# Performance work log

Measured on AMD Instinct MI355X. Metric: run time of the kernel, lower is better.

Reference implementation:

```python
import jax, jax.numpy as jnp
import numpy as np

B, T, E, H = 64, 200, 512, 8
D = E // H          # head size 64
SCALE = E ** -0.5   # NOTE: original scales by EMBED_DIM**-0.5, not head_size**-0.5


def _ln(x, g, b):
    mu = jnp.mean(x, axis=-1, keepdims=True)
    d = x - mu
    v = jnp.mean(d * d, axis=-1, keepdims=True)
    return g * d * jax.lax.rsqrt(v + 1e-5) + b


def _forward(idx, memory, src_mask, pred_mask,
             sa_wq, sa_wk, sa_wv, sa_wo, sa_bo,
             ca_wq, ca_wk, ca_wv, ca_wo, ca_bo,
             f_w1, f_b1, f_w2, f_b2,
             ln1_g, ln1_b, ln2_g, ln2_b, ln3_g, ln3_b):
    causal = jnp.tril(jnp.ones((T, T), dtype=bool))      # [T,T]
    pm = (pred_mask != 0)[:, None, :, None]              # [B,1,T,1]
    sm = (src_mask != 0)[:, None, :, None]               # [B,1,T,1]

    # --- masked multi-head self-attention (query AND key zeroed by pred_mask) ---
    h = _ln(idx, ln1_g, ln1_b)
    q = jnp.where(pm, jnp.einsum('bte,hed->bhtd', h, sa_wq), 0.0)
    k = jnp.where(pm, jnp.einsum('bte,hed->bhtd', h, sa_wk), 0.0)
    v = jnp.einsum('bte,hed->bhtd', h, sa_wv)
    s = jnp.einsum('bhtd,bhsd->bhts', q, k) * SCALE
    s = jnp.where(causal, s, -jnp.inf)
    w = jax.nn.softmax(s, axis=-1)
    o = jnp.einsum('bhts,bhsd->bthd', w, v).reshape(B, T, E)
    idx = o @ sa_wo + sa_bo + idx

    # --- cross-attention: keys from memory (src-masked), VALUES FROM x (per original code) ---
    h = _ln(idx, ln2_g, ln2_b)
    q = jnp.einsum('bte,hed->bhtd', h, ca_wq)
    k = jnp.where(sm, jnp.einsum('bse,hed->bhsd', memory, ca_wk), 0.0)
    v = jnp.einsum('bte,hed->bhtd', h, ca_wv)
    s = jnp.einsum('bhtd,bhsd->bhts', q, k) * SCALE
    s = jnp.where(causal, s, -jnp.inf)   # mask=True in Decoder's ca
    w = jax.nn.softmax(s, axis=-1)
    o = jnp.einsum('bhts,bhsd->bthd', w, v).reshape(B, T, E)
    idx = o @ ca_wo + ca_bo + idx

    # --- feed-forward ---
    h = _ln(idx, ln3_g, ln3_b)
    idx = jax.nn.relu(h @ f_w1 + f_b1) @ f_w2 + f_b2 + idx
    return idx


def setup_inputs() -> dict:
    key = jax.random.key(0)
    ks = jax.random.split(key, 20)
    nrm = lambda k, sh: jax.random.normal(k, sh, jnp.float32) * 0.02
    return {
        'idx': jax.random.normal(ks[0], (B, T, E), jnp.float32),
        'memory': jax.random.normal(ks[1], (B, T, E), jnp.float32),
        'src_mask': jax.random.randint(ks[2], (B, T), 0, 2, jnp.int32),
        'pred_mask': jax.random.randint(ks[3], (B, T), 0, 2, jnp.int32),
        'sa_wq': nrm(ks[4], (H, E, D)), 'sa_wk': nrm(ks[5], (H, E, D)),
        'sa_wv': nrm(ks[6], (H, E, D)),
        'sa_wo': nrm(ks[7], (E, E)), 'sa_bo': jnp.zeros((E,), jnp.float32),
        'ca_wq': nrm(ks[8], (H, E, D)), 'ca_wk': nrm(ks[9], (H, E, D)),
        'ca_wv': nrm(ks[10], (H, E, D)),
        'ca_wo': nrm(ks[11], (E, E)), 'ca_bo': jnp.zeros((E,), jnp.float32),
        'f_w1': nrm(ks[12], (E, 4 * E)), 'f_b1': jnp.zeros((4 * E,), jnp.float32),
        'f_w2': nrm(ks[13], (4 * E, E)), 'f_b2': jnp.zeros((E,), jnp.float32),
        'ln1_g': jnp.ones((E,), jnp.float32), 'ln1_b': jnp.zeros((E,), jnp.float32),
        'ln2_g': jnp.ones((E,), jnp.float32), 'ln2_b': jnp.zeros((E,), jnp.float32),
        'ln3_g': jnp.ones((E,), jnp.float32), 'ln3_b': jnp.zeros((E,), jnp.float32),
    }


def reference(idx, memory, src_mask, pred_mask,
              sa_wq, sa_wk, sa_wv, sa_wo, sa_bo,
              ca_wq, ca_wk, ca_wv, ca_wo, ca_bo,
              f_w1, f_b1, f_w2, f_b2,
              ln1_g, ln1_b, ln2_g, ln2_b, ln3_g, ln3_b):
    return _forward(idx, memory, src_mask, pred_mask,
                    sa_wq, sa_wk, sa_wv, sa_wo, sa_bo,
                    ca_wq, ca_wk, ca_wv, ca_wo, ca_bo,
                    f_w1, f_b1, f_w2, f_b2,
                    ln1_g, ln1_b, ln2_g, ln2_b, ln3_g, ln3_b)
```

## Files before the change

kernel.cpp:

```cpp
#include <hip/hip_runtime.h>
#include <hip/hip_bf16.h>

#define B_ 64
#define T_ 200
#define E_ 512
#define H_ 8
#define D_ 64

static constexpr float SCALE = 0.044194173824159216f;

typedef __attribute__((ext_vector_type(8))) short bf16x8;
typedef __attribute__((ext_vector_type(4))) short bf16x4;
typedef __attribute__((ext_vector_type(4))) float f32x4;

static __device__ inline short f2bf(float f) {
    __hip_bfloat16 h = __float2bfloat16(f);
    return *(short*)&h;
}

static __device__ __forceinline__ void gload16(const short* g, short* l) {
    __builtin_amdgcn_global_load_lds(
        (const __attribute__((address_space(1))) void*)g,
        (__attribute__((address_space(3))) void*)l, 16, 0, 0);
}

__global__ void conv_kernel(const float* __restrict__ in,
                            __hip_bfloat16* __restrict__ out, int n) {
    int i = (blockIdx.x * blockDim.x + threadIdx.x) * 4;
    if (i < n) {
        f32x4 v = *(const f32x4*)(in + i);
        bf16x4 r;
        #pragma unroll
        for (int j = 0; j < 4; ++j) r[j] = f2bf(v[j]);
        *(bf16x4*)((short*)out + i) = r;
    }
}

template <int MODE>
__global__ __launch_bounds__(256) void wt_kernel(const float* __restrict__ in,
                                                 __hip_bfloat16* __restrict__ out,
                                                 int N, int K) {
    __shared__ float tile[64][65];
    int n0 = blockIdx.x * 64, k0 = blockIdx.y * 64;
    int tx = threadIdx.x & 63, ty = threadIdx.x >> 6;
    #pragma unroll
    for (int i = 0; i < 16; ++i) {
        int k = k0 + ty + i * 4;
        float v;
        if (MODE == 0) {
            v = in[(size_t)k * N + n0 + tx];
        } else {
            int h = n0 >> 6;
            v = in[((size_t)h * K + k) * 64 + tx];
        }
        tile[ty + i * 4][tx] = v;
    }
    __syncthreads();
    #pragma unroll
    for (int i = 0; i < 16; ++i) {
        int n = ty + i * 4;
        out[(size_t)(n0 + n) * K + k0 + tx] = __float2bfloat16(tile[tx][n]);
    }
}

__global__ __launch_bounds__(256) void ln_kernel(const float* __restrict__ x,
                                                 const float* __restrict__ g,
                                                 const float* __restrict__ bta,
                                                 __hip_bfloat16* __restrict__ out) {
    __shared__ float red[4];
    int row = blockIdx.x;
    const float* xr = x + (size_t)row * E_;
    int tid = threadIdx.x;
    float v0 = xr[tid], v1 = xr[tid + 256];
    float s = v0 + v1;
    for (int off = 32; off; off >>= 1) s += __shfl_down(s, off, 64);
    if ((tid & 63) == 0) red[tid >> 6] = s;
    __syncthreads();
    float mu = (red[0] + red[1] + red[2] + red[3]) * (1.0f / E_);
    __syncthreads();
    float d0 = v0 - mu, d1 = v1 - mu;
    float sq = d0 * d0 + d1 * d1;
    for (int off = 32; off; off >>= 1) sq += __shfl_down(sq, off, 64);
    if ((tid & 63) == 0) red[tid >> 6] = sq;
    __syncthreads();
    float var = (red[0] + red[1] + red[2] + red[3]) * (1.0f / E_);
    float r = rsqrtf(var + 1e-5f);
    out[(size_t)row * E_ + tid] = __float2bfloat16(g[tid] * d0 * r + bta[tid]);
    out[(size_t)row * E_ + tid + 256] =
        __float2bfloat16(g[tid + 256] * d1 * r + bta[tid + 256]);
}

template <int MSK, int RELU, int OM, int RES, int BIAS>
__global__ __launch_bounds__(256) void mgemm_kernel(
    const short* __restrict__ A, const short* __restrict__ BT,
    const float* __restrict__ bias, const int* __restrict__ rmask,
    const float* __restrict__ resid, void* __restrict__ Cv,
    int M, int N, int K, size_t wstep) {
    __shared__ __align__(16) short As[2][128 * 32];
    __shared__ __align__(16) short Bs[2][128 * 32];
    int tid = threadIdx.x;
    int wave = tid >> 6, lane = tid & 63;
    int qq = lane >> 4, l15 = lane & 15;

    int nwg = gridDim.x * gridDim.y;
    int flat = blockIdx.y * gridDim.x + blockIdx.x;
    int xcd = flat & 7, bix = flat >> 3;
    int qw = nwg >> 3, rw = nwg & 7;
    int nf = (xcd < rw ? xcd * (qw + 1) : rw * (qw + 1) + (xcd - rw) * qw) + bix;
    int by = nf / gridDim.x, bx = nf - by * gridDim.x;
    int m0 = by * 128, n0 = bx * 128;
    int wm = (wave & 1) * 64, wn = (wave >> 1) * 64;

    int srow = lane >> 2;
    int scol = ((lane & 3) ^ ((srow >> 1) & 3)) * 8;
    const short* gA = A + (size_t)(m0 + wave * 32 + srow) * K + scol;
    const short* gB = BT + (size_t)(n0 + wave * 32 + srow) * K + scol;
    int lofs = wave * 1024;
    size_t rstep = (size_t)16 * K;

    int swz = (qq ^ ((l15 >> 1) & 3)) * 8;

    f32x4 acc[4][4] = {};

    gload16(gA, &As[0][lofs]);
    gload16(gA + rstep, &As[0][lofs + 512]);
    gload16(gB, &Bs[0][lofs]);
    gload16(gB + rstep, &Bs[0][lofs + 512]);

    int nk = K >> 5;
    for (int it = 0; it < nk; ++it) {
        int cur = it & 1;
        if (it + 1 < nk) {
            int k1 = (it + 1) << 5;
            int nxt = cur ^ 1;
            gload16(gA + k1, &As[nxt][lofs]);
            gload16(gA + k1 + rstep, &As[nxt][lofs + 512]);
            gload16(gB + k1, &Bs[nxt][lofs]);
            gload16(gB + k1 + rstep, &Bs[nxt][lofs + 512]);
            asm volatile("s_waitcnt vmcnt(4)" ::: "memory");
        } else {
            asm volatile("s_waitcnt vmcnt(0)" ::: "memory");
        }
        __builtin_amdgcn_s_barrier();
        bf16x8 af[4], bfr[4];
        #pragma unroll
        for (int i = 0; i < 4; ++i)
            af[i] = *(bf16x8*)(&As[cur][(wm + i * 16 + l15) * 32 + swz]);
        #pragma unroll
        for (int j = 0; j < 4; ++j)
            bfr[j] = *(bf16x8*)(&Bs[cur][(wn + j * 16 + l15) * 32 + swz]);
        #pragma unroll
        for (int i = 0; i < 4; ++i)
            #pragma unroll
            for (int j = 0; j < 4; ++j)
                acc[i][j] = __builtin_amdgcn_mfma_f32_16x16x32_bf16(
                    af[i], bfr[j], acc[i][j], 0, 0, 0);
        asm volatile("" ::: "memory");
        __builtin_amdgcn_s_barrier();
    }

    #pragma unroll
    for (int i = 0; i < 4; ++i) {
        #pragma unroll
        for (int r = 0; r < 4; ++r) {
            int row = m0 + wm + i * 16 + qq * 4 + r;
            float mval = 1.0f;
            if (MSK) mval = (rmask[row] != 0) ? 1.0f : 0.0f;
            #pragma unroll
            for (int j = 0; j < 4; ++j) {
                int col = n0 + wn + j * 16 + l15;
                float val = acc[i][j][r];
                if (BIAS) val += bias[col];
                if (MSK == 1) val *= mval;
                if (MSK == 2) { if (col < 1024) val *= mval; }
                if (RELU) val = fmaxf(val, 0.0f);
                if (RES) val += resid[(size_t)row * N + col];
                if (OM == 0) {
                    ((float*)Cv)[(size_t)row * N + col] = val;
                } else if (OM == 1) {
                    int b_ = row / T_, t = row - b_ * T_;
                    int hh = col >> 6, d = col & 63;
                    ((__hip_bfloat16*)Cv)[(((size_t)b_ * H_ + hh) * T_ + t) * D_ + d] =
                        __float2bfloat16(val);
                } else if (OM == 3) {
                    int b_ = row / T_, t = row - b_ * T_;
                    int which = col >> 9, cc = col & 511;
                    int hh = cc >> 6, d = cc & 63;
                    ((__hip_bfloat16*)Cv)[(size_t)which * wstep +
                                          (((size_t)b_ * H_ + hh) * T_ + t) * D_ + d] =
                        __float2bfloat16(val);
                } else {
                    ((__hip_bfloat16*)Cv)[(size_t)row * N + col] =
                        __float2bfloat16(val);
                }
            }
        }
    }
}

#define NQT 13
__global__ __launch_bounds__(256) void fattn_kernel(const short* __restrict__ q,
                                                    const short* __restrict__ k,
                                                    const short* __restrict__ v,
                                                    __hip_bfloat16* __restrict__ o) {
    __shared__ __align__(16) short Kf[NQT * 8 * 16 * 8];
    __shared__ __align__(16) short Vf[4 * 28 * 16 * 8];
    __shared__ __align__(16) short Pb[4 * 512];

    int tid = threadIdx.x;
    int wave = tid >> 6, lane = tid & 63;
    int qq = lane >> 4, l15 = lane & 15;
    int bh = blockIdx.x;
    int b = bh >> 3, h = bh & 7;

    const short* kp = k + (size_t)bh * T_ * D_;
    const short* vp = v + (size_t)bh * T_ * D_;
    const short* qp = q + (size_t)bh * T_ * D_;

    for (int idx = tid; idx < 8 * 208; idx += 256) {
        int g = idx / 208, s = idx - g * 208;
        int kt = s >> 4, l = s & 15;
        bf16x8 val;
        if (s < 200) {
            val = *(const bf16x8*)(kp + (size_t)s * 64 + g * 8);
        } else {
            #pragma unroll
            for (int j = 0; j < 8; ++j) val[j] = 0;
        }
        *(bf16x8*)&Kf[((kt * 8 + g) * 16 + l) * 8] = val;
    }
    for (int idx = tid; idx < 28 * 64; idx += 256) {
        int g = idx >> 6, d = idx & 63;
        int nt = d >> 4, dl = d & 15;
        bf16x8 val;
        if (g < 25) {
            #pragma unroll
            for (int j = 0; j < 8; ++j) val[j] = vp[(g * 8 + j) * 64 + d];
        } else {
            #pragma unroll
            for (int j = 0; j < 8; ++j) val[j] = 0;
        }
        *(bf16x8*)&Vf[((nt * 28 + g) * 16 + dl) * 8] = val;
    }
    __syncthreads();

    short* pb = &Pb[wave * 512];

    for (int qt = wave; qt < NQT; qt += 4) {
        int t0 = qt * 16;
        bf16x8 qf[2];
        #pragma unroll
        for (int ks = 0; ks < 2; ++ks)
            qf[ks] = *(const bf16x8*)(qp + (size_t)(t0 + l15) * 64 + ks * 32 + qq * 8);
        f32x4 sc[NQT];
        #pragma unroll
        for (int kt = 0; kt < NQT; ++kt) {
            f32x4 a = {0.f, 0.f, 0.f, 0.f};
            bf16x8 kf0 = *(const bf16x8*)&Kf[((kt * 8 + qq) * 16 + l15) * 8];
            bf16x8 kf1 = *(const bf16x8*)&Kf[((kt * 8 + 4 + qq) * 16 + l15) * 8];
            a = __builtin_amdgcn_mfma_f32_16x16x32_bf16(qf[0], kf0, a, 0, 0, 0);
            a = __builtin_amdgcn_mfma_f32_16x16x32_bf16(qf[1], kf1, a, 0, 0, 0);
            sc[kt] = a;
        }
        #pragma unroll
        for (int kt = 0; kt < NQT; ++kt) {
            #pragma unroll
            for (int r = 0; r < 4; ++r) {
                int col = kt * 16 + l15;
                int rowg = t0 + qq * 4 + r;
                sc[kt][r] = (col <= rowg) ? sc[kt][r] * SCALE : -1e30f;
            }
        }
        float mx[4], sum[4], inv[4];
        #pragma unroll
        for (int r = 0; r < 4; ++r) {
            float m = -1e30f;
            #pragma unroll
            for (int kt = 0; kt < NQT; ++kt) m = fmaxf(m, sc[kt][r]);
            #pragma unroll
            for (int off = 1; off < 16; off <<= 1)
                m = fmaxf(m, __shfl_xor(m, off, 64));
            mx[r] = m;
        }
        #pragma unroll
        for (int r = 0; r < 4; ++r) sum[r] = 0.f;
        #pragma unroll
        for (int kt = 0; kt < NQT; ++kt) {
            #pragma unroll
            for (int r = 0; r < 4; ++r) {
                float e = __expf(sc[kt][r] - mx[r]);
                sc[kt][r] = e;
                sum[r] += e;
            }
        }
        #pragma unroll
        for (int r = 0; r < 4; ++r) {
            float s = sum[r];
            #pragma unroll
            for (int off = 1; off < 16; off <<= 1) s += __shfl_xor(s, off, 64);
            inv[r] = 1.0f / s;
        }
        f32x4 oa[4] = {};
        #pragma unroll
        for (int c = 0; c < 7; ++c) {
            #pragma unroll
            for (int kt2 = 0; kt2 < 2; ++kt2) {
                int kt = c * 2 + kt2;
                int g = kt2 * 2 + (l15 >> 3);
                int jj = l15 & 7;
                #pragma unroll
                for (int r = 0; r < 4; ++r) {
                    float val = (kt < NQT) ? sc[kt][r] : 0.0f;
                    pb[(g * 16 + qq * 4 + r) * 8 + jj] = f2bf(val);
                }
            }
            bf16x8 pf = *(const bf16x8*)&pb[(qq * 16 + l15) * 8];
            #pragma unroll
            for (int nt = 0; nt < 4; ++nt) {
                bf16x8 vf = *(const bf16x8*)&Vf[((nt * 28 + c * 4 + qq) * 16 + l15) * 8];
                oa[nt] = __builtin_amdgcn_mfma_f32_16x16x32_bf16(pf, vf, oa[nt], 0, 0, 0);
            }
        }
        #pragma unroll
        for (int nt = 0; nt < 4; ++nt) {
            #pragma unroll
            for (int r = 0; r < 4; ++r) {
                int t = t0 + qq * 4 + r;
                if (t < T_) {
                    int d = nt * 16 + l15;
                    o[((size_t)b * T_ + t) * E_ + h * D_ + d] =
                        __float2bfloat16(oa[nt][r] * inv[r]);
                }
            }
        }
    }
}

extern "C" void kernel_launch(void* const* d_in, const int* in_sizes, int n_in,
                              void* d_out, int out_size, void* d_ws, size_t ws_size,
                              hipStream_t stream) {
    const float* idx    = (const float*)d_in[0];
    const float* memory = (const float*)d_in[1];
    const int* src_mask  = (const int*)d_in[2];
    const int* pred_mask = (const int*)d_in[3];
    const float* sa_wq = (const float*)d_in[4];
    const float* sa_wk = (const float*)d_in[5];
    const float* sa_wv = (const float*)d_in[6];
    const float* sa_wo = (const float*)d_in[7];
    const float* sa_bo = (const float*)d_in[8];
    const float* ca_wq = (const float*)d_in[9];
    const float* ca_wk = (const float*)d_in[10];
    const float* ca_wv = (const float*)d_in[11];
    const float* ca_wo = (const float*)d_in[12];
    const float* ca_bo = (const float*)d_in[13];
    const float* f_w1  = (const float*)d_in[14];
    const float* f_b1  = (const float*)d_in[15];
    const float* f_w2  = (const float*)d_in[16];
    const float* f_b2  = (const float*)d_in[17];
    const float* ln1_g = (const float*)d_in[18];
    const float* ln1_b = (const float*)d_in[19];
    const float* ln2_g = (const float*)d_in[20];
    const float* ln2_b = (const float*)d_in[21];
    const float* ln3_g = (const float*)d_in[22];
    const float* ln3_b = (const float*)d_in[23];
    float* out = (float*)d_out;

    const size_t BTE = (size_t)B_ * T_ * E_;
    const size_t EE = (size_t)E_ * E_;

    char* p = (char*)d_ws;
    short* qb = (short*)p;            p += BTE * 2;
    short* kb = (short*)p;            p += BTE * 2;
    short* vb = (short*)p;            p += BTE * 2;
    float* x1 = (float*)p;            p += BTE * 4;
    __hip_bfloat16* h_bf   = (__hip_bfloat16*)p; p += BTE * 2;
    __hip_bfloat16* o_bf   = (__hip_bfloat16*)p; p += BTE * 2;
    __hip_bfloat16* mem_bf = (__hip_bfloat16*)p; p += BTE * 2;
    __hip_bfloat16* w_qkv_s = (__hip_bfloat16*)p; p += 3 * EE * 2;
    __hip_bfloat16* w_o_s   = (__hip_bfloat16*)p; p += EE * 2;
    __hip_bfloat16* w_qv_c  = (__hip_bfloat16*)p; p += 2 * EE * 2;
    __hip_bfloat16* w_k_c   = (__hip_bfloat16*)p; p += EE * 2;
    __hip_bfloat16* w_o_c   = (__hip_bfloat16*)p; p += EE * 2;
    __hip_bfloat16* w1T     = (__hip_bfloat16*)p; p += EE * 4 * 2;
    __hip_bfloat16* w2T     = (__hip_bfloat16*)p; p += EE * 4 * 2;
    short* ff_bf = qb;

    const int M = B_ * T_;
    dim3 blk(256);
    dim3 g512(E_ / 128, M / 128);
    dim3 g1024(8, M / 128);
    dim3 g1536(12, M / 128);
    dim3 g2048(16, M / 128);

    dim3 t512(8, 8), t_w1(32, 8), t_w2(8, 32);
    wt_kernel<1><<<t512, blk, 0, stream>>>(sa_wq, w_qkv_s, E_, E_);
    wt_kernel<1><<<t512, blk, 0, stream>>>(sa_wk, w_qkv_s + EE, E_, E_);
    wt_kernel<1><<<t512, blk, 0, stream>>>(sa_wv, w_qkv_s + 2 * EE, E_, E_);
    wt_kernel<0><<<t512, blk, 0, stream>>>(sa_wo, w_o_s, E_, E_);
    wt_kernel<1><<<t512, blk, 0, stream>>>(ca_wq, w_qv_c, E_, E_);
    wt_kernel<1><<<t512, blk, 0, stream>>>(ca_wv, w_qv_c + EE, E_, E_);
    wt_kernel<1><<<t512, blk, 0, stream>>>(ca_wk, w_k_c, E_, E_);
    wt_kernel<0><<<t512, blk, 0, stream>>>(ca_wo, w_o_c, E_, E_);
    wt_kernel<0><<<t_w1, blk, 0, stream>>>(f_w1, w1T, 4 * E_, E_);
    wt_kernel<0><<<t_w2, blk, 0, stream>>>(f_w2, w2T, E_, 4 * E_);
    conv_kernel<<<((int)(BTE / 4) + 255) / 256, 256, 0, stream>>>(memory, mem_bf,
                                                                  (int)BTE);

    ln_kernel<<<M, 256, 0, stream>>>(idx, ln1_g, ln1_b, h_bf);
    mgemm_kernel<2,0,3,0,0><<<g1536, blk, 0, stream>>>(
        (const short*)h_bf, (const short*)w_qkv_s, nullptr, pred_mask, nullptr,
        qb, M, 3 * E_, E_, BTE);
    fattn_kernel<<<B_ * H_, 256, 0, stream>>>(qb, kb, vb, o_bf);
    mgemm_kernel<0,0,0,1,1><<<g512, blk, 0, stream>>>(
        (const short*)o_bf, (const short*)w_o_s, sa_bo, nullptr, idx, x1,
        M, E_, E_, 0);

    ln_kernel<<<M, 256, 0, stream>>>(x1, ln2_g, ln2_b, h_bf);
    mgemm_kernel<0,0,3,0,0><<<g1024, blk, 0, stream>>>(
        (const short*)h_bf, (const short*)w_qv_c, nullptr, nullptr, nullptr,
        qb, M, 2 * E_, E_, 2 * BTE);
    mgemm_kernel<1,0,1,0,0><<<g512, blk, 0, stream>>>(
        (const short*)mem_bf, (const short*)w_k_c, nullptr, src_mask, nullptr,
        kb, M, E_, E_, 0);
    fattn_kernel<<<B_ * H_, 256, 0, stream>>>(qb, kb, vb, o_bf);
    mgemm_kernel<0,0,0,1,1><<<g512, blk, 0, stream>>>(
        (const short*)o_bf, (const short*)w_o_c, ca_bo, nullptr, x1, out,
        M, E_, E_, 0);

    ln_kernel<<<M, 256, 0, stream>>>(out, ln3_g, ln3_b, h_bf);
    mgemm_kernel<0,1,2,0,1><<<g2048, blk, 0, stream>>>(
        (const short*)h_bf, (const short*)w1T, f_b1, nullptr, nullptr,
        ff_bf, M, 4 * E_, E_, 0);
    mgemm_kernel<0,0,0,1,1><<<g512, blk, 0, stream>>>(
        (const short*)ff_bf, (const short*)w2T, f_b2, nullptr, out, out,
        M, E_, 4 * E_, 0);
}
```

Baseline: 458.0 us.

## Widen GEMM K-tile to 64 and fuse cross-attention Q/V/K projections into one launch

The GEMM kernel now stages 64-wide K slices per iteration instead of 32, with an 8-way XOR swizzle for LDS and twice the shared memory per block. This halves the number of barrier/wait iterations and issues more loads per stage. Separately, the cross-attention Q/V projection and the memory-side K projection are merged into a single 1536-column GEMM. Columns at or above 1024 select the memory input, apply the src mask and route output to the K buffer. This removes one launch and improves grid fill, at the cost of higher LDS use (64KB per block), which may reduce occupancy.

```diff
diff --git a/kernel.cpp b/kernel.cpp
--- a/kernel.cpp
+++ b/kernel.cpp
@@ -92,12 +92,13 @@
 
 template <int MSK, int RELU, int OM, int RES, int BIAS>
 __global__ __launch_bounds__(256) void mgemm_kernel(
-    const short* __restrict__ A, const short* __restrict__ BT,
+    const short* __restrict__ A, const short* __restrict__ A2,
+    const short* __restrict__ BT,
     const float* __restrict__ bias, const int* __restrict__ rmask,
     const float* __restrict__ resid, void* __restrict__ Cv,
     int M, int N, int K, size_t wstep) {
-    __shared__ __align__(16) short As[2][128 * 32];
-    __shared__ __align__(16) short Bs[2][128 * 32];
+    __shared__ __align__(16) short As[2][128 * 64];
+    __shared__ __align__(16) short Bs[2][128 * 64];
     int tid = threadIdx.x;
     int wave = tid >> 6, lane = tid & 63;
     int qq = lane >> 4, l15 = lane & 15;
@@ -111,50 +112,58 @@
     int m0 = by * 128, n0 = bx * 128;
     int wm = (wave & 1) * 64, wn = (wave >> 1) * 64;
 
-    int srow = lane >> 2;
-    int scol = ((lane & 3) ^ ((srow >> 1) & 3)) * 8;
-    const short* gA = A + (size_t)(m0 + wave * 32 + srow) * K + scol;
+    const short* Ap = A;
+    if (OM == 4 && n0 >= 1024) Ap = A2;
+
+    int srow = lane >> 3;
+    int scol = ((lane & 7) ^ srow) * 8;
+    const short* gA = Ap + (size_t)(m0 + wave * 32 + srow) * K + scol;
     const short* gB = BT + (size_t)(n0 + wave * 32 + srow) * K + scol;
-    int lofs = wave * 1024;
-    size_t rstep = (size_t)16 * K;
-
-    int swz = (qq ^ ((l15 >> 1) & 3)) * 8;
+    int lofs = wave * 32 * 64;
+    size_t rstep = (size_t)8 * K;
 
     f32x4 acc[4][4] = {};
 
-    gload16(gA, &As[0][lofs]);
-    gload16(gA + rstep, &As[0][lofs + 512]);
-    gload16(gB, &Bs[0][lofs]);
-    gload16(gB + rstep, &Bs[0][lofs + 512]);
-
-    int nk = K >> 5;
+    auto STAGE = [&](int kt, int bufi) {
+        int kk = kt << 6;
+        #pragma unroll
+        for (int c = 0; c < 4; ++c) {
+            gload16(gA + kk + c * rstep, &As[bufi][lofs + c * 512]);
+            gload16(gB + kk + c * rstep, &Bs[bufi][lofs + c * 512]);
+        }
+    };
+
+    int nk = K >> 6;
+    STAGE(0, 0);
+
     for (int it = 0; it < nk; ++it) {
         int cur = it & 1;
         if (it + 1 < nk) {
-            int k1 = (it + 1) << 5;
-            int nxt = cur ^ 1;
-            gload16(gA + k1, &As[nxt][lofs]);
-            gload16(gA + k1 + rstep, &As[nxt][lofs + 512]);
-            gload16(gB + k1, &Bs[nxt][lofs]);
-            gload16(gB + k1 + rstep, &Bs[nxt][lofs + 512]);
-            asm volatile("s_waitcnt vmcnt(4)" ::: "memory");
+            STAGE(it + 1, cur ^ 1);
+            asm volatile("s_waitcnt vmcnt(8)" ::: "memory");
         } else {
             asm volatile("s_waitcnt vmcnt(0)" ::: "memory");
         }
         __builtin_amdgcn_s_barrier();
-        bf16x8 af[4], bfr[4];
-        #pragma unroll
-        for (int i = 0; i < 4; ++i)
-            af[i] = *(bf16x8*)(&As[cur][(wm + i * 16 + l15) * 32 + swz]);
-        #pragma unroll
-        for (int j = 0; j < 4; ++j)
-            bfr[j] = *(bf16x8*)(&Bs[cur][(wn + j * 16 + l15) * 32 + swz]);
-        #pragma unroll
-        for (int i = 0; i < 4; ++i)
+        bf16x8 af[2][4], bfr[2][4];
+        #pragma unroll
+        for (int ks = 0; ks < 2; ++ks) {
+            int pu = ((ks * 4 + qq) ^ (l15 & 7)) * 8;
+            #pragma unroll
+            for (int i = 0; i < 4; ++i)
+                af[ks][i] = *(bf16x8*)(&As[cur][(wm + i * 16 + l15) * 64 + pu]);
             #pragma unroll
             for (int j = 0; j < 4; ++j)
-                acc[i][j] = __builtin_amdgcn_mfma_f32_16x16x32_bf16(
-                    af[i], bfr[j], acc[i][j], 0, 0, 0);
+                bfr[ks][j] = *(bf16x8*)(&Bs[cur][(wn + j * 16 + l15) * 64 + pu]);
+        }
+        #pragma unroll
+        for (int ks = 0; ks < 2; ++ks)
+            #pragma unroll
+            for (int i = 0; i < 4; ++i)
+                #pragma unroll
+                for (int j = 0; j < 4; ++j)
+                    acc[i][j] = __builtin_amdgcn_mfma_f32_16x16x32_bf16(
+                        af[ks][i], bfr[ks][j], acc[i][j], 0, 0, 0);
         asm volatile("" ::: "memory");
         __builtin_amdgcn_s_barrier();
     }
@@ -173,20 +182,24 @@
                 if (BIAS) val += bias[col];
                 if (MSK == 1) val *= mval;
                 if (MSK == 2) { if (col < 1024) val *= mval; }
+                if (MSK == 3) { if (col >= 1024) val *= mval; }
                 if (RELU) val = fmaxf(val, 0.0f);
                 if (RES) val += resid[(size_t)row * N + col];
                 if (OM == 0) {
                     ((float*)Cv)[(size_t)row * N + col] = val;
-                } else if (OM == 1) {
-                    int b_ = row / T_, t = row - b_ * T_;
-                    int hh = col >> 6, d = col & 63;
-                    ((__hip_bfloat16*)Cv)[(((size_t)b_ * H_ + hh) * T_ + t) * D_ + d] =
-                        __float2bfloat16(val);
                 } else if (OM == 3) {
                     int b_ = row / T_, t = row - b_ * T_;
                     int which = col >> 9, cc = col & 511;
                     int hh = cc >> 6, d = cc & 63;
                     ((__hip_bfloat16*)Cv)[(size_t)which * wstep +
+                                          (((size_t)b_ * H_ + hh) * T_ + t) * D_ + d] =
+                        __float2bfloat16(val);
+                } else if (OM == 4) {
+                    int b_ = row / T_, t = row - b_ * T_;
+                    int which = col >> 9, cc = col & 511;
+                    size_t off = (which == 1) ? 2 * wstep : (which == 2 ? wstep : 0);
+                    int hh = cc >> 6, d = cc & 63;
+                    ((__hip_bfloat16*)Cv)[off +
                                           (((size_t)b_ * H_ + hh) * T_ + t) * D_ + d] =
                         __float2bfloat16(val);
                 } else {
@@ -378,8 +391,7 @@
     __hip_bfloat16* mem_bf = (__hip_bfloat16*)p; p += BTE * 2;
     __hip_bfloat16* w_qkv_s = (__hip_bfloat16*)p; p += 3 * EE * 2;
     __hip_bfloat16* w_o_s   = (__hip_bfloat16*)p; p += EE * 2;
-    __hip_bfloat16* w_qv_c  = (__hip_bfloat16*)p; p += 2 * EE * 2;
-    __hip_bfloat16* w_k_c   = (__hip_bfloat16*)p; p += EE * 2;
+    __hip_bfloat16* w_qvk_c = (__hip_bfloat16*)p; p += 3 * EE * 2;
     __hip_bfloat16* w_o_c   = (__hip_bfloat16*)p; p += EE * 2;
     __hip_bfloat16* w1T     = (__hip_bfloat16*)p; p += EE * 4 * 2;
     __hip_bfloat16* w2T     = (__hip_bfloat16*)p; p += EE * 4 * 2;
@@ -388,7 +400,6 @@
     const int M = B_ * T_;
     dim3 blk(256);
     dim3 g512(E_ / 128, M / 128);
-    dim3 g1024(8, M / 128);
     dim3 g1536(12, M / 128);
     dim3 g2048(16, M / 128);
 
@@ -397,9 +408,9 @@
     wt_kernel<1><<<t512, blk, 0, stream>>>(sa_wk, w_qkv_s + EE, E_, E_);
     wt_kernel<1><<<t512, blk, 0, stream>>>(sa_wv, w_qkv_s + 2 * EE, E_, E_);
     wt_kernel<0><<<t512, blk, 0, stream>>>(sa_wo, w_o_s, E_, E_);
-    wt_kernel<1><<<t512, blk, 0, stream>>>(ca_wq, w_qv_c, E_, E_);
-    wt_kernel<1><<<t512, blk, 0, stream>>>(ca_wv, w_qv_c + EE, E_, E_);
-    wt_kernel<1><<<t512, blk, 0, stream>>>(ca_wk, w_k_c, E_, E_);
+    wt_kernel<1><<<t512, blk, 0, stream>>>(ca_wq, w_qvk_c, E_, E_);
+    wt_kernel<1><<<t512, blk, 0, stream>>>(ca_wv, w_qvk_c + EE, E_, E_);
+    wt_kernel<1><<<t512, blk, 0, stream>>>(ca_wk, w_qvk_c + 2 * EE, E_, E_);
     wt_kernel<0><<<t512, blk, 0, stream>>>(ca_wo, w_o_c, E_, E_);
     wt_kernel<0><<<t_w1, blk, 0, stream>>>(f_w1, w1T, 4 * E_, E_);
     wt_kernel<0><<<t_w2, blk, 0, stream>>>(f_w2, w2T, E_, 4 * E_);
@@ -408,30 +419,27 @@
 
     ln_kernel<<<M, 256, 0, stream>>>(idx, ln1_g, ln1_b, h_bf);
     mgemm_kernel<2,0,3,0,0><<<g1536, blk, 0, stream>>>(
-        (const short*)h_bf, (const short*)w_qkv_s, nullptr, pred_mask, nullptr,
-        qb, M, 3 * E_, E_, BTE);
+        (const short*)h_bf, nullptr, (const short*)w_qkv_s, nullptr, pred_mask,
+        nullptr, qb, M, 3 * E_, E_, BTE);
     fattn_kernel<<<B_ * H_, 256, 0, stream>>>(qb, kb, vb, o_bf);
     mgemm_kernel<0,0,0,1,1><<<g512, blk, 0, stream>>>(
-        (const short*)o_bf, (const short*)w_o_s, sa_bo, nullptr, idx, x1,
+        (const short*)o_bf, nullptr, (const short*)w_o_s, sa_bo, nullptr, idx, x1,
         M, E_, E_, 0);
 
     ln_kernel<<<M, 256, 0, stream>>>(x1, ln2_g, ln2_b, h_bf);
-    mgemm_kernel<0,0,3,0,0><<<g1024, blk, 0, stream>>>(
-        (const short*)h_bf, (const short*)w_qv_c, nullptr, nullptr, nullptr,
-        qb, M, 2 * E_, E_, 2 * BTE);
-    mgemm_kernel<1,0,1,0,0><<<g512, blk, 0, stream>>>(
-        (const short*)mem_bf, (const short*)w_k_c, nullptr, src_mask, nullptr,
-        kb, M, E_, E_, 0);
+    mgemm_kernel<3,0,4,0,0><<<g1536, blk, 0, stream>>>(
+        (const short*)h_bf, (const short*)mem_bf, (const short*)w_qvk_c, nullptr,
+        src_mask, nullptr, qb, M, 3 * E_, E_, BTE);
     fattn_kernel<<<B_ * H_, 256, 0, stream>>>(qb, kb, vb, o_bf);
     mgemm_kernel<0,0,0,1,1><<<g512, blk, 0, stream>>>(
-        (const short*)o_bf, (const short*)w_o_c, ca_bo, nullptr, x1, out,
+        (const short*)o_bf, nullptr, (const short*)w_o_c, ca_bo, nullptr, x1, out,
         M, E_, E_, 0);
 
     ln_kernel<<<M, 256, 0, stream>>>(out, ln3_g, ln3_b, h_bf);
     mgemm_kernel<0,1,2,0,1><<<g2048, blk, 0, stream>>>(
-        (const short*)h_bf, (const short*)w1T, f_b1, nullptr, nullptr,
+        (const short*)h_bf, nullptr, (const short*)w1T, f_b1, nullptr, nullptr,
         ff_bf, M, 4 * E_, E_, 0);
     mgemm_kernel<0,0,0,1,1><<<g512, blk, 0, stream>>>(
-        (const short*)ff_bf, (const short*)w2T, f_b2, nullptr, out, out,
+        (const short*)ff_bf, nullptr, (const short*)w2T, f_b2, nullptr, out, out,
         M, E_, 4 * E_, 0);
 }
```

After: 435.3 us. 4.9% less time.
